# Kernel optimization log

Measured on AMD Instinct MI355X. Metric: run time of the kernel, lower is better.

Reference implementation:

```python
import jax, jax.numpy as jnp
import numpy as np

B, S = 32, 128          # batch, seq_len
C, K = 256, 128         # num_concept, dim_k (== dim_e == dim_correct)
DC = 128                # dim_correct
NQ, NIT, NUT = 10000, 1024, 1024


def _xavier(k, shape):
    fan_out, fan_in = shape[0], shape[1]
    bound = float(np.sqrt(6.0 / (fan_in + fan_out)))
    return jax.random.uniform(k, shape, jnp.float32, -bound, bound)


def setup_inputs() -> dict:
    key = jax.random.key(0)
    ks = jax.random.split(key, 16)
    question_seq = jax.random.randint(ks[0], (B, S), 0, NQ + 1)
    interval_time_seq = jax.random.randint(ks[1], (B, S), 0, NIT + 1)
    use_time_seq = jax.random.randint(ks[2], (B, S), 0, NUT + 1)
    correct_seq = jnp.round(jax.random.uniform(ks[3], (B, S))).astype(jnp.float32)
    E_q = _xavier(ks[4], (NQ + 1, K))
    E_it = _xavier(ks[5], (NIT + 1, K))
    E_ut = _xavier(ks[6], (NUT + 1, K))
    q_matrix = (jax.random.uniform(ks[7], (NQ + 1, C)) < 0.03).astype(jnp.float32)
    h0 = _xavier(ks[8], (C, K))  # xavier init of the initial concept memory
    W1 = _xavier(ks[9], (K, K + K + DC)); b1 = jnp.zeros((K,), jnp.float32)
    W2 = _xavier(ks[10], (K, 4 * K));     b2 = jnp.zeros((K,), jnp.float32)
    W3 = _xavier(ks[11], (K, 4 * K));     b3 = jnp.zeros((K,), jnp.float32)
    W4 = _xavier(ks[12], (K, 3 * K));     b4 = jnp.zeros((K,), jnp.float32)
    W5 = _xavier(ks[13], (K, 2 * K));     b5 = jnp.zeros((K,), jnp.float32)
    return dict(question_seq=question_seq, interval_time_seq=interval_time_seq,
                use_time_seq=use_time_seq, correct_seq=correct_seq,
                E_q=E_q, E_it=E_it, E_ut=E_ut, q_matrix=q_matrix, h0=h0,
                W1=W1, b1=b1, W2=W2, b2=b2, W3=W3, b3=b3,
                W4=W4, b4=b4, W5=W5, b5=b5)


def _forward(question_seq, interval_time_seq, use_time_seq, correct_seq,
             E_q, E_it, E_ut, q_matrix, h0,
             W1, b1, W2, b2, W3, b3, W4, b4, W5, b5):
    bsz, slen = question_seq.shape
    dim_k = h0.shape[1]
    dim_c = W1.shape[1] - 2 * dim_k

    q_emb = E_q[question_seq]            # [B,S,K]
    it_emb = E_it[interval_time_seq]     # [B,S,K]
    ut_emb = E_ut[use_time_seq]          # [B,S,K]
    c_emb = jnp.broadcast_to(correct_seq[..., None], (bsz, slen, dim_c))
    all_learning = jnp.concatenate([q_emb, ut_emb, c_emb], -1) @ W1.T + b1  # [B,S,K]
    qe = q_matrix[question_seq]          # [B,S,C]

    h_pre0 = jnp.tile(h0[None], (bsz, 1, 1))                     # [B,C,K]
    h_tilde0 = jnp.einsum('bc,bck->bk', qe[:, 0], h_pre0)        # q_e @ h at t=0
    learning0 = jnp.zeros((bsz, dim_k), all_learning.dtype)

    # split linear_4 weight over its (h_pre, LG, it) concat blocks
    W4h, W4l, W4i = W4[:, :dim_k], W4[:, dim_k:2 * dim_k], W4[:, 2 * dim_k:]

    # time-major per-step inputs for t = 0 .. S-2
    xs = (jnp.swapaxes(it_emb[:, :-1], 0, 1),
          jnp.swapaxes(all_learning[:, :-1], 0, 1),
          jnp.swapaxes(qe[:, :-1], 0, 1),
          jnp.swapaxes(qe[:, 1:], 0, 1),
          jnp.swapaxes(q_emb[:, 1:], 0, 1))

    def step(carry, x):
        h_pre, h_tilde_pre, learning_pre = carry
        it, learning, qe_t, qe_n, qemb_n = x
        cat = jnp.concatenate([learning_pre, it, learning, h_tilde_pre], -1)  # [B,4K]
        learning_gain = jnp.tanh(cat @ W2.T + b2)
        gamma_l = jax.nn.sigmoid(cat @ W3.T + b3)
        LG = gamma_l * (learning_gain + 1.0) * 0.5                 # [B,K]
        LG_tilde = qe_t[:, :, None] * LG[:, None, :]               # [B,C,K] outer write
        gamma_f = jax.nn.sigmoid(jnp.einsum('bck,jk->bcj', h_pre, W4h)
                                 + (LG @ W4l.T + it @ W4i.T + b4)[:, None, :])
        h = LG_tilde + gamma_f * h_pre                             # [B,C,K]
        h_tilde = jnp.einsum('bc,bck->bk', qe_n, h)                # read for t+1
        y = jax.nn.sigmoid(jnp.concatenate([qemb_n, h_tilde], -1) @ W5.T + b5).sum(-1) / dim_k
        return (h, h_tilde, learning), y

    _, ys = jax.lax.scan(step, (h_pre0, h_tilde0, learning0), xs)  # ys: [S-1,B]
    pred = jnp.concatenate([jnp.zeros((bsz, 1), ys.dtype), ys.T], axis=1)
    return pred


def reference(question_seq, interval_time_seq, use_time_seq, correct_seq,
              E_q, E_it, E_ut, q_matrix, h0,
              W1, b1, W2, b2, W3, b3, W4, b4, W5, b5):
    return _forward(question_seq, interval_time_seq, use_time_seq, correct_seq,
                    E_q, E_it, E_ut, q_matrix, h0,
                    W1, b1, W2, b2, W3, b3, W4, b4, W5, b5)
```

## Files before the change

kernel.cpp:

```cpp
#include <hip/hip_runtime.h>
#include <hip/hip_bf16.h>


typedef __bf16 bf16x8 __attribute__((ext_vector_type(8)));
typedef __bf16 bf16x4 __attribute__((ext_vector_type(4)));
typedef float f32x4 __attribute__((ext_vector_type(4)));

#define HBIDX(c,k) ((((c)<<7)) + ((k) ^ (((c)&15)<<3)))

__device__ __forceinline__ float sigmf(float x){
  return __builtin_amdgcn_rcpf(1.0f + __expf(-x));
}

__device__ __forceinline__ bf16x8 cvt8(float4 a, float4 b){
  bf16x8 r;
  r[0]=(__bf16)a.x; r[1]=(__bf16)a.y; r[2]=(__bf16)a.z; r[3]=(__bf16)a.w;
  r[4]=(__bf16)b.x; r[5]=(__bf16)b.y; r[6]=(__bf16)b.z; r[7]=(__bf16)b.w;
  return r;
}

__device__ __forceinline__ void mk_hilo(float4 a, float4 b, bf16x8& hi, bf16x8& lo){
  float v[8] = {a.x,a.y,a.z,a.w,b.x,b.y,b.z,b.w};
  #pragma unroll
  for (int i = 0; i < 8; i++){
    __bf16 h = (__bf16)v[i];
    hi[i] = h;
    lo[i] = (__bf16)(v[i] - (float)h);
  }
}

__device__ __forceinline__ f32x4 mfma16(bf16x8 a, bf16x8 b, f32x4 c){
  return __builtin_amdgcn_mfma_f32_16x16x32_bf16(a, b, c, 0, 0, 0);
}

__global__ __launch_bounds__(256) void k1_al(
    const int* __restrict__ qseq, const int* __restrict__ utseq,
    const float* __restrict__ corr,
    const float* __restrict__ Eq, const float* __restrict__ Eut,
    const float* __restrict__ W1, const float* __restrict__ b1,
    const float* __restrict__ W5, const float* __restrict__ b5,
    float* __restrict__ AL, float* __restrict__ pre5)
{
  __shared__ __bf16 inA[64*256];
  __shared__ float corrs[64];
  __shared__ float b1s[128], b5s[128], rsp[256];
  const int tid = threadIdx.x, blk = blockIdx.x;
  if (tid < 128){ b1s[tid]=b1[tid]; b5s[tid]=b5[tid]; }
  {
    int j = tid & 127, hf = tid >> 7;
    const float* p = W1 + j*384 + 256 + hf*64;
    float s = 0.f;
    for (int i = 0; i < 64; i++) s += p[i];
    rsp[tid] = s;
  }
  {
    int r = tid >> 2, seg = tid & 3;
    int R = blk*64 + r;
    int qi = qseq[R], ui = utseq[R];
    if (seg == 0) corrs[r] = corr[R];
    for (int i = 0; i < 64; i++){
      int col = seg*64 + i;
      float v = (col < 128) ? Eq[qi*128 + col] : Eut[ui*128 + (col-128)];
      inA[((r*256 + col) ^ ((r&7)<<3))] = (__bf16)v;
    }
  }
  __syncthreads();
  const int w = tid >> 6, lane = tid & 63;
  const int la = lane & 15, g = lane >> 4;
  const int rbase = w*16;
  bf16x8 af[8];
  #pragma unroll
  for (int kt = 0; kt < 8; kt++){
    int idx = ((rbase+la)*256 + kt*32 + g*8) ^ ((la&7)<<3);
    af[kt] = *(const bf16x8*)&inA[idx];
  }
  for (int jt = 0; jt < 8; jt++){
    f32x4 acc = {0.f,0.f,0.f,0.f};
    const float* Wb = W1 + (jt*16+la)*384;
    #pragma unroll
    for (int kt = 0; kt < 8; kt++){
      const float* p = Wb + kt*32 + g*8;
      acc = mfma16(af[kt], cvt8(*(const float4*)p, *(const float4*)(p+4)), acc);
    }
    int j = jt*16 + la;
    float rsj = rsp[j] + rsp[j+128];
    #pragma unroll
    for (int rr = 0; rr < 4; rr++){
      int row = rbase + g*4 + rr;
      int R = blk*64 + row;
      AL[R*128 + j] = acc[rr] + b1s[j] + corrs[row]*rsj;
    }
  }
  for (int jt = 0; jt < 8; jt++){
    f32x4 acc = {0.f,0.f,0.f,0.f};
    const float* Wb = W5 + (jt*16+la)*256;
    #pragma unroll
    for (int kt = 0; kt < 4; kt++){
      const float* p = Wb + kt*32 + g*8;
      acc = mfma16(af[kt], cvt8(*(const float4*)p, *(const float4*)(p+4)), acc);
    }
    int j = jt*16 + la;
    #pragma unroll
    for (int rr = 0; rr < 4; rr++){
      int row = rbase + g*4 + rr;
      int R = blk*64 + row;
      pre5[R*128 + j] = acc[rr] + b5s[j];
    }
  }
}

__global__ __launch_bounds__(256) void k2_pre(
    const int* __restrict__ itseq, const float* __restrict__ Eit,
    const float* __restrict__ AL,
    const float* __restrict__ W2, const float* __restrict__ W3,
    const float* __restrict__ W4,
    const float* __restrict__ b2, const float* __restrict__ b3,
    const float* __restrict__ b4,
    float* __restrict__ pre23, float* __restrict__ pre4)
{
  __shared__ __bf16 inA[64*384];
  __shared__ int obase[64];
  __shared__ float b2s[128], b3s[128], b4s[128];
  const int tid = threadIdx.x, blk = blockIdx.x;
  if (tid < 128){ b2s[tid]=b2[tid]; b3s[tid]=b3[tid]; b4s[tid]=b4[tid]; }
  {
    int r = tid >> 2, seg = tid & 3;
    int R = blk*64 + r;
    bool valid = (R < 4064);
    int b_ = R / 127, tau = R % 127;
    if (seg == 0) obase[r] = valid ? (b_*127 + tau) : -1;
    int itv = valid ? itseq[b_*128 + tau] : 0;
    for (int i = 0; i < 96; i++){
      int col = seg*96 + i;
      float v = 0.f;
      if (valid){
        if (col < 128)      v = (tau > 0) ? AL[(b_*128 + tau-1)*128 + col] : 0.f;
        else if (col < 256) v = Eit[itv*128 + (col-128)];
        else                v = AL[(b_*128 + tau)*128 + (col-256)];
      }
      inA[((r*384 + col) ^ ((r&7)<<3))] = (__bf16)v;
    }
  }
  __syncthreads();
  const int w = tid >> 6, lane = tid & 63;
  const int la = lane & 15, g = lane >> 4;
  const int rbase = w*16;
  bf16x8 af[12];
  #pragma unroll
  for (int kt = 0; kt < 12; kt++){
    int idx = ((rbase+la)*384 + kt*32 + g*8) ^ ((la&7)<<3);
    af[kt] = *(const bf16x8*)&inA[idx];
  }
  for (int jt = 0; jt < 16; jt++){
    f32x4 acc = {0.f,0.f,0.f,0.f};
    int j = jt*16 + la;
    const float* Wb = (j < 128) ? (W2 + j*512) : (W3 + (j-128)*512);
    #pragma unroll
    for (int kt = 0; kt < 12; kt++){
      const float* p = Wb + kt*32 + g*8;
      acc = mfma16(af[kt], cvt8(*(const float4*)p, *(const float4*)(p+4)), acc);
    }
    float bias = (j < 128) ? b2s[j] : b3s[j-128];
    #pragma unroll
    for (int rr = 0; rr < 4; rr++){
      int row = rbase + g*4 + rr;
      int ob = obase[row];
      if (ob >= 0) pre23[ob*256 + j] = acc[rr] + bias;
    }
  }
  for (int jt = 0; jt < 8; jt++){
    f32x4 acc = {0.f,0.f,0.f,0.f};
    int j = jt*16 + la;
    const float* Wb = W4 + j*384 + 256;
    #pragma unroll
    for (int kk = 0; kk < 4; kk++){
      const float* p = Wb + kk*32 + g*8;
      acc = mfma16(af[4+kk], cvt8(*(const float4*)p, *(const float4*)(p+4)), acc);
    }
    #pragma unroll
    for (int rr = 0; rr < 4; rr++){
      int row = rbase + g*4 + rr;
      int ob = obase[row];
      if (ob >= 0) pre4[ob*128 + j] = acc[rr] + b4s[j];
    }
  }
}

#define SCAN_LDS_BYTES (34944*4)

__global__ __launch_bounds__(512, 2) void lpkt_scan(
    const float* __restrict__ qmat, const int* __restrict__ qseq,
    const float* __restrict__ h0,
    const float* __restrict__ W2, const float* __restrict__ W3,
    const float* __restrict__ W4,
    const float* __restrict__ pre23, const float* __restrict__ pre4,
    float* __restrict__ hist)
{
  extern __shared__ float lds[];
  __bf16* hB  = (__bf16*)lds;
  float* htb0 = lds + 32768;
  float* htb1 = lds + 32896;
  float* LGb  = lds + 33024;
  float* zb   = lds + 33152;
  float* qeb  = lds + 33280;
  float* p23L = lds + 34048;
  float* p4L  = lds + 34560;
  int*   qsl  = (int*)(lds + 34816);

  const int tid  = threadIdx.x;
  const int b    = blockIdx.x;
  const int lane = tid & 63;
  const int w    = tid >> 6;
  const int la   = lane & 15, g = lane >> 4;
  const int jq   = w & 3;
  const int ch   = w >> 2;

  bf16x8 af[2][4];
  #pragma unroll
  for (int jj = 0; jj < 2; jj++){
    #pragma unroll
    for (int kt = 0; kt < 4; kt++){
      const float* p = W4 + ((jq*2+jj)*16+la)*384 + kt*32 + g*8;
      af[jj][kt] = cvt8(*(const float4*)p, *(const float4*)(p+4));
    }
  }
  bf16x8 af23[2][4];
  bf16x8 af4l[4];
  #pragma unroll
  for (int kt = 0; kt < 4; kt++){
    const float* p2 = W2 + (w*16+la)*512 + 384 + kt*32 + g*8;
    const float* p3 = W3 + (w*16+la)*512 + 384 + kt*32 + g*8;
    const float* p4 = W4 + (w*16+la)*384 + 128 + kt*32 + g*8;
    af23[0][kt] = cvt8(*(const float4*)p2, *(const float4*)(p2+4));
    af23[1][kt] = cvt8(*(const float4*)p3, *(const float4*)(p3+4));
    af4l[kt]    = cvt8(*(const float4*)p4, *(const float4*)(p4+4));
  }

  if (tid < 128) qsl[tid] = qseq[b*128 + tid];
  __syncthreads();
  const float* pre23b = pre23 + b*127*256;
  const float* pre4b  = pre4  + b*127*128;
  if (tid < 64)       *(float4*)&qeb[tid*4] = *(const float4*)(qmat + (size_t)qsl[0]*256 + tid*4);
  else if (tid < 128) *(float4*)&qeb[256 + (tid-64)*4] = *(const float4*)(qmat + (size_t)qsl[1]*256 + (tid-64)*4);
  else if (tid < 192) *(float4*)&p23L[(tid-128)*4] = *(const float4*)(pre23b + (tid-128)*4);
  else if (tid < 224) *(float4*)&p4L[(tid-192)*4]  = *(const float4*)(pre4b  + (tid-192)*4);
  else if (tid < 256){ float4 z4i = {0.f,0.f,0.f,0.f}; *(float4*)&htb0[(tid-224)*4] = z4i; }

  float4 hreg[8][2];
  #pragma unroll
  for (int cg = 0; cg < 8; cg++){
    const int c_ = ch*128 + cg*16 + la;
    #pragma unroll
    for (int jj = 0; jj < 2; jj++){
      const int k0 = (jq*2+jj)*16 + g*4;
      float4 v = *(const float4*)(h0 + c_*128 + k0);
      hreg[cg][jj] = v;
      bf16x4 hb; hb[0]=(__bf16)v.x; hb[1]=(__bf16)v.y; hb[2]=(__bf16)v.z; hb[3]=(__bf16)v.w;
      *(bf16x4*)&hB[HBIDX(c_, k0)] = hb;
    }
  }
  __syncthreads();
  #pragma unroll
  for (int cg = 0; cg < 8; cg++){
    const int c_ = ch*128 + cg*16 + la;
    float q = qeb[c_];
    if (q != 0.f){
      #pragma unroll
      for (int jj = 0; jj < 2; jj++){
        const int k0 = (jq*2+jj)*16 + g*4;
        float4 hv = hreg[cg][jj];
        atomicAdd(&htb0[k0+0], q*hv.x);
        atomicAdd(&htb0[k0+1], q*hv.y);
        atomicAdd(&htb0[k0+2], q*hv.z);
        atomicAdd(&htb0[k0+3], q*hv.w);
      }
    }
  }
  __syncthreads();

  int i0 = 0, i1 = 1, i2 = 2;

  for (int tau = 0; tau < 127; tau++){
    float* htc = (tau & 1) ? htb1 : htb0;
    float* htn = (tau & 1) ? htb0 : htb1;
    float* qec = qeb + i0*256;
    float* qen = qeb + i1*256;
    float* qep = qeb + i2*256;
    const float* p23c = p23L + (tau & 1)*256;
    const float* p4c  = p4L  + (tau & 1)*128;
    const __bf16* hBr = hB + (tau & 1)*32768;
    __bf16*       hBw = hB + ((tau+1) & 1)*32768;

    if (tid < 128) htn[tid] = 0.f;
    {
      bf16x8 xh[4], xl[4];
      #pragma unroll
      for (int kt = 0; kt < 4; kt++){
        int k0 = kt*32 + g*8;
        mk_hilo(*(const float4*)&htc[k0], *(const float4*)&htc[k0+4], xh[kt], xl[kt]);
      }
      f32x4 aLh = {0.f,0.f,0.f,0.f}, aLl = {0.f,0.f,0.f,0.f};
      f32x4 aGh = {0.f,0.f,0.f,0.f}, aGl = {0.f,0.f,0.f,0.f};
      #pragma unroll
      for (int kt = 0; kt < 4; kt++){
        aLh = mfma16(af23[0][kt], xh[kt], aLh);
        aLl = mfma16(af23[0][kt], xl[kt], aLl);
        aGh = mfma16(af23[1][kt], xh[kt], aGh);
        aGl = mfma16(af23[1][kt], xl[kt], aGl);
      }
      if (la == 0){
        float4 lp4 = *(const float4*)&p23c[w*16 + g*4];
        float4 gp4 = *(const float4*)&p23c[128 + w*16 + g*4];
        float4 LG4;
        LG4.x = sigmf(aGh[0]+aGl[0]+gp4.x) * sigmf(2.f*(aLh[0]+aLl[0]+lp4.x));
        LG4.y = sigmf(aGh[1]+aGl[1]+gp4.y) * sigmf(2.f*(aLh[1]+aLl[1]+lp4.y));
        LG4.z = sigmf(aGh[2]+aGl[2]+gp4.z) * sigmf(2.f*(aLh[2]+aLl[2]+lp4.z));
        LG4.w = sigmf(aGh[3]+aGl[3]+gp4.w) * sigmf(2.f*(aLh[3]+aLl[3]+lp4.w));
        *(float4*)&LGb[w*16 + g*4] = LG4;
      }
    }
    __syncthreads();

    {
      bf16x8 lh[4];
      #pragma unroll
      for (int kt = 0; kt < 4; kt++){
        int k0 = kt*32 + g*8;
        lh[kt] = cvt8(*(const float4*)&LGb[k0], *(const float4*)&LGb[k0+4]);
      }
      f32x4 az0 = {0.f,0.f,0.f,0.f}, az1 = {0.f,0.f,0.f,0.f};
      az0 = mfma16(af4l[0], lh[0], az0);
      az1 = mfma16(af4l[1], lh[1], az1);
      az0 = mfma16(af4l[2], lh[2], az0);
      az1 = mfma16(af4l[3], lh[3], az1);
      if (la == 0){
        float4 zp = *(const float4*)&p4c[w*16 + g*4];
        float4 zv = {az0[0]+az1[0]+zp.x, az0[1]+az1[1]+zp.y,
                     az0[2]+az1[2]+zp.z, az0[3]+az1[3]+zp.w};
        *(float4*)&zb[w*16 + g*4] = zv;
      }
    }
    __syncthreads();

    float4 pf23, pf4, pfqe;
    const bool dopf = (tau < 126);
    const bool do23 = dopf && (tid < 64);
    const bool do4  = dopf && (tid >= 64) && (tid < 96);
    const bool doqe = dopf && (tid >= 448);
    if (do23) pf23 = *(const float4*)(pre23b + (tau+1)*256 + tid*4);
    if (do4)  pf4  = *(const float4*)(pre4b  + (tau+1)*128 + (tid-64)*4);
    if (doqe) pfqe = *(const float4*)(qmat + (size_t)qsl[tau+2]*256 + (tid-448)*4);

    float4 z4[2], lg4[2];
    #pragma unroll
    for (int jj = 0; jj < 2; jj++){
      const int k0 = (jq*2+jj)*16 + g*4;
      z4[jj]  = *(const float4*)&zb[k0];
      lg4[jj] = *(const float4*)&LGb[k0];
    }

    #pragma unroll
    for (int cg = 0; cg < 8; cg++){
      const int c_ = ch*128 + cg*16 + la;
      bf16x8 bfv[4];
      #pragma unroll
      for (int kt = 0; kt < 4; kt++)
        bfv[kt] = *(const bf16x8*)&hBr[HBIDX(c_, kt*32 + g*8)];
      const float qe_t = qec[c_], qe_n = qen[c_];
      const bool nz = (qe_n != 0.f);
      #pragma unroll
      for (int jj = 0; jj < 2; jj++){
        f32x4 acc = {0.f,0.f,0.f,0.f};
        #pragma unroll
        for (int kt = 0; kt < 4; kt++)
          acc = mfma16(af[jj][kt], bfv[kt], acc);
        const int k0 = (jq*2+jj)*16 + g*4;
        float4 hp = hreg[cg][jj];
        float4 hn;
        hn.x = qe_t*lg4[jj].x + sigmf(acc[0] + z4[jj].x)*hp.x;
        hn.y = qe_t*lg4[jj].y + sigmf(acc[1] + z4[jj].y)*hp.y;
        hn.z = qe_t*lg4[jj].z + sigmf(acc[2] + z4[jj].z)*hp.z;
        hn.w = qe_t*lg4[jj].w + sigmf(acc[3] + z4[jj].w)*hp.w;
        hreg[cg][jj] = hn;
        bf16x4 hb; hb[0]=(__bf16)hn.x; hb[1]=(__bf16)hn.y; hb[2]=(__bf16)hn.z; hb[3]=(__bf16)hn.w;
        *(bf16x4*)&hBw[HBIDX(c_, k0)] = hb;
        if (nz){
          atomicAdd(&htn[k0+0], qe_n*hn.x);
          atomicAdd(&htn[k0+1], qe_n*hn.y);
          atomicAdd(&htn[k0+2], qe_n*hn.z);
          atomicAdd(&htn[k0+3], qe_n*hn.w);
        }
      }
    }
    if (do23) *(float4*)&p23L[((tau+1)&1)*256 + tid*4] = pf23;
    if (do4)  *(float4*)&p4L[((tau+1)&1)*128 + (tid-64)*4] = pf4;
    if (doqe) *(float4*)&qep[(tid-448)*4] = pfqe;
    __syncthreads();

    if (tid < 32){
      float4 v = *(const float4*)&htn[tid*4];
      *(float4*)(hist + ((size_t)b*127 + tau)*128 + tid*4) = v;
    }
    int t_ = i0; i0 = i1; i1 = i2; i2 = t_;
  }
}

__global__ __launch_bounds__(128) void k4_y(
    const float* __restrict__ hist, const float* __restrict__ pre5,
    const float* __restrict__ W5, float* __restrict__ out)
{
  const int R = blockIdx.x;
  const int s = R & 127, b = R >> 7;
  const int j = threadIdx.x;
  __shared__ float xs[128];
  __shared__ float partial[2];
  if (s == 0){ if (j == 0) out[R] = 0.f; return; }
  xs[j] = hist[((size_t)b*127 + (s-1))*128 + j];
  __syncthreads();
  const float* wr = W5 + j*256 + 128;
  float acc = pre5[(size_t)R*128 + j];
  #pragma unroll
  for (int k = 0; k < 128; k += 4){
    float4 wv = *(const float4*)&wr[k];
    float4 xv = *(const float4*)&xs[k];
    acc += wv.x*xv.x + wv.y*xv.y + wv.z*xv.z + wv.w*xv.w;
  }
  float v = sigmf(acc);
  #pragma unroll
  for (int m = 1; m < 64; m <<= 1) v += __shfl_xor(v, m);
  if ((j & 63) == 0) partial[j >> 6] = v;
  __syncthreads();
  if (j == 0) out[R] = (partial[0] + partial[1]) * (1.f/128.f);
}

extern "C" void kernel_launch(void* const* d_in, const int* in_sizes, int n_in,
                              void* d_out, int out_size, void* d_ws, size_t ws_size,
                              hipStream_t stream) {
  const int*   qseq  = (const int*)  d_in[0];
  const int*   itseq = (const int*)  d_in[1];
  const int*   utseq = (const int*)  d_in[2];
  const float* corr  = (const float*)d_in[3];
  const float* Eq    = (const float*)d_in[4];
  const float* Eit   = (const float*)d_in[5];
  const float* Eut   = (const float*)d_in[6];
  const float* qmat  = (const float*)d_in[7];
  const float* h0    = (const float*)d_in[8];
  const float* W1    = (const float*)d_in[9];
  const float* b1    = (const float*)d_in[10];
  const float* W2    = (const float*)d_in[11];
  const float* b2    = (const float*)d_in[12];
  const float* W3    = (const float*)d_in[13];
  const float* b3    = (const float*)d_in[14];
  const float* W4    = (const float*)d_in[15];
  const float* b4    = (const float*)d_in[16];
  const float* W5    = (const float*)d_in[17];
  const float* b5    = (const float*)d_in[18];
  float* out = (float*)d_out;

  float* ws    = (float*)d_ws;
  float* AL    = ws;
  float* hist  = ws;
  float* pre5  = ws + 524288;
  float* pre23 = ws + 1048576;
  float* pre4  = ws + 2088960;

  (void)hipFuncSetAttribute(reinterpret_cast<const void*>(&lpkt_scan),
                            hipFuncAttributeMaxDynamicSharedMemorySize,
                            SCAN_LDS_BYTES);

  hipLaunchKernelGGL(k1_al, dim3(64), dim3(256), 0, stream,
                     qseq, utseq, corr, Eq, Eut, W1, b1, W5, b5, AL, pre5);
  hipLaunchKernelGGL(k2_pre, dim3(64), dim3(256), 0, stream,
                     itseq, Eit, AL, W2, W3, W4, b2, b3, b4, pre23, pre4);
  hipLaunchKernelGGL(lpkt_scan, dim3(32), dim3(512), SCAN_LDS_BYTES, stream,
                     qmat, qseq, h0, W2, W3, W4, pre23, pre4, hist);
  hipLaunchKernelGGL(k4_y, dim3(4096), dim3(128), 0, stream,
                     hist, pre5, W5, out);
}
```

Before: 903.7 us.

## Remove a barrier per scan step and reduce h_tilde via shuffles

The z = W4l·LG matvec no longer runs as its own phase behind a barrier. Each wave now computes its own slice of z redundantly from a bf16 copy of LG, which drops one __syncthreads per timestep. The per-element atomicAdds into h_tilde, previously made only for nonzero q entries, are replaced by register accumulation, a 16-lane xor-shuffle reduction and a few atomics per wave. This costs extra MFMA work, extra weight registers and shuffles every step in exchange for fewer barriers and less LDS atomic contention.

Result: no change. 904.1 us (+0.0%).

```diff
diff --git a/kernel.cpp b/kernel.cpp
--- a/kernel.cpp
+++ b/kernel.cpp
@@ -31,6 +31,16 @@
 
 __device__ __forceinline__ f32x4 mfma16(bf16x8 a, bf16x8 b, f32x4 c){
   return __builtin_amdgcn_mfma_f32_16x16x32_bf16(a, b, c, 0, 0, 0);
+}
+
+__device__ __forceinline__ void red16(f32x4& r){
+  #pragma unroll
+  for (int m = 1; m < 16; m <<= 1){
+    r[0] += __shfl_xor(r[0], m);
+    r[1] += __shfl_xor(r[1], m);
+    r[2] += __shfl_xor(r[2], m);
+    r[3] += __shfl_xor(r[3], m);
+  }
 }
 
 __global__ __launch_bounds__(256) void k1_al(
@@ -186,7 +196,7 @@
   }
 }
 
-#define SCAN_LDS_BYTES (34944*4)
+#define SCAN_LDS_BYTES (34880*4)
 
 __global__ __launch_bounds__(512, 2) void lpkt_scan(
     const float* __restrict__ qmat, const int* __restrict__ qseq,
@@ -198,14 +208,14 @@
 {
   extern __shared__ float lds[];
   __bf16* hB  = (__bf16*)lds;
-  float* htb0 = lds + 32768;
-  float* htb1 = lds + 32896;
-  float* LGb  = lds + 33024;
-  float* zb   = lds + 33152;
-  float* qeb  = lds + 33280;
-  float* p23L = lds + 34048;
-  float* p4L  = lds + 34560;
-  int*   qsl  = (int*)(lds + 34816);
+  float*  htb0 = lds + 32768;
+  float*  htb1 = lds + 32896;
+  float*  LGb  = lds + 33024;
+  __bf16* LGh  = (__bf16*)(lds + 33152);
+  float*  qeb  = lds + 33216;
+  float*  p23L = lds + 33984;
+  float*  p4L  = lds + 34496;
+  int*    qsl  = (int*)(lds + 34752);
 
   const int tid  = threadIdx.x;
   const int b    = blockIdx.x;
@@ -216,24 +226,24 @@
   const int ch   = w >> 2;
 
   bf16x8 af[2][4];
+  bf16x8 af4l[2][4];
   #pragma unroll
   for (int jj = 0; jj < 2; jj++){
     #pragma unroll
     for (int kt = 0; kt < 4; kt++){
-      const float* p = W4 + ((jq*2+jj)*16+la)*384 + kt*32 + g*8;
-      af[jj][kt] = cvt8(*(const float4*)p, *(const float4*)(p+4));
+      const float* ph = W4 + ((jq*2+jj)*16+la)*384 + kt*32 + g*8;
+      const float* pl = W4 + ((jq*2+jj)*16+la)*384 + 128 + kt*32 + g*8;
+      af[jj][kt]   = cvt8(*(const float4*)ph, *(const float4*)(ph+4));
+      af4l[jj][kt] = cvt8(*(const float4*)pl, *(const float4*)(pl+4));
     }
   }
   bf16x8 af23[2][4];
-  bf16x8 af4l[4];
   #pragma unroll
   for (int kt = 0; kt < 4; kt++){
     const float* p2 = W2 + (w*16+la)*512 + 384 + kt*32 + g*8;
     const float* p3 = W3 + (w*16+la)*512 + 384 + kt*32 + g*8;
-    const float* p4 = W4 + (w*16+la)*384 + 128 + kt*32 + g*8;
     af23[0][kt] = cvt8(*(const float4*)p2, *(const float4*)(p2+4));
     af23[1][kt] = cvt8(*(const float4*)p3, *(const float4*)(p3+4));
-    af4l[kt]    = cvt8(*(const float4*)p4, *(const float4*)(p4+4));
   }
 
   if (tid < 128) qsl[tid] = qseq[b*128 + tid];
@@ -260,20 +270,23 @@
     }
   }
   __syncthreads();
-  #pragma unroll
-  for (int cg = 0; cg < 8; cg++){
-    const int c_ = ch*128 + cg*16 + la;
-    float q = qeb[c_];
-    if (q != 0.f){
-      #pragma unroll
-      for (int jj = 0; jj < 2; jj++){
-        const int k0 = (jq*2+jj)*16 + g*4;
-        float4 hv = hreg[cg][jj];
-        atomicAdd(&htb0[k0+0], q*hv.x);
-        atomicAdd(&htb0[k0+1], q*hv.y);
-        atomicAdd(&htb0[k0+2], q*hv.z);
-        atomicAdd(&htb0[k0+3], q*hv.w);
-      }
+  {
+    f32x4 r0 = {0.f,0.f,0.f,0.f}, r1 = {0.f,0.f,0.f,0.f};
+    #pragma unroll
+    for (int cg = 0; cg < 8; cg++){
+      const int c_ = ch*128 + cg*16 + la;
+      float q = qeb[c_];
+      float4 h0v = hreg[cg][0], h1v = hreg[cg][1];
+      r0[0] += q*h0v.x; r0[1] += q*h0v.y; r0[2] += q*h0v.z; r0[3] += q*h0v.w;
+      r1[0] += q*h1v.x; r1[1] += q*h1v.y; r1[2] += q*h1v.z; r1[3] += q*h1v.w;
+    }
+    red16(r0); red16(r1);
+    if (la == 0){
+      const int k0 = (jq*2)*16 + g*4, k1 = (jq*2+1)*16 + g*4;
+      atomicAdd(&htb0[k0+0], r0[0]); atomicAdd(&htb0[k0+1], r0[1]);
+      atomicAdd(&htb0[k0+2], r0[2]); atomicAdd(&htb0[k0+3], r0[3]);
+      atomicAdd(&htb0[k1+0], r1[0]); atomicAdd(&htb0[k1+1], r1[1]);
+      atomicAdd(&htb0[k1+2], r1[2]); atomicAdd(&htb0[k1+3], r1[3]);
     }
   }
   __syncthreads();
@@ -308,36 +321,19 @@
         aGh = mfma16(af23[1][kt], xh[kt], aGh);
         aGl = mfma16(af23[1][kt], xl[kt], aGl);
       }
+      float4 lp4 = *(const float4*)&p23c[w*16 + g*4];
+      float4 gp4 = *(const float4*)&p23c[128 + w*16 + g*4];
+      float4 LG4;
+      LG4.x = sigmf(aGh[0]+aGl[0]+gp4.x) * sigmf(2.f*(aLh[0]+aLl[0]+lp4.x));
+      LG4.y = sigmf(aGh[1]+aGl[1]+gp4.y) * sigmf(2.f*(aLh[1]+aLl[1]+lp4.y));
+      LG4.z = sigmf(aGh[2]+aGl[2]+gp4.z) * sigmf(2.f*(aLh[2]+aLl[2]+lp4.z));
+      LG4.w = sigmf(aGh[3]+aGl[3]+gp4.w) * sigmf(2.f*(aLh[3]+aLl[3]+lp4.w));
       if (la == 0){
-        float4 lp4 = *(const float4*)&p23c[w*16 + g*4];
-        float4 gp4 = *(const float4*)&p23c[128 + w*16 + g*4];
-        float4 LG4;
-        LG4.x = sigmf(aGh[0]+aGl[0]+gp4.x) * sigmf(2.f*(aLh[0]+aLl[0]+lp4.x));
-        LG4.y = sigmf(aGh[1]+aGl[1]+gp4.y) * sigmf(2.f*(aLh[1]+aLl[1]+lp4.y));
-        LG4.z = sigmf(aGh[2]+aGl[2]+gp4.z) * sigmf(2.f*(aLh[2]+aLl[2]+lp4.z));
-        LG4.w = sigmf(aGh[3]+aGl[3]+gp4.w) * sigmf(2.f*(aLh[3]+aLl[3]+lp4.w));
         *(float4*)&LGb[w*16 + g*4] = LG4;
-      }
-    }
-    __syncthreads();
-
-    {
-      bf16x8 lh[4];
-      #pragma unroll
-      for (int kt = 0; kt < 4; kt++){
-        int k0 = kt*32 + g*8;
-        lh[kt] = cvt8(*(const float4*)&LGb[k0], *(const float4*)&LGb[k0+4]);
-      }
-      f32x4 az0 = {0.f,0.f,0.f,0.f}, az1 = {0.f,0.f,0.f,0.f};
-      az0 = mfma16(af4l[0], lh[0], az0);
-      az1 = mfma16(af4l[1], lh[1], az1);
-      az0 = mfma16(af4l[2], lh[2], az0);
-      az1 = mfma16(af4l[3], lh[3], az1);
-      if (la == 0){
-        float4 zp = *(const float4*)&p4c[w*16 + g*4];
-        float4 zv = {az0[0]+az1[0]+zp.x, az0[1]+az1[1]+zp.y,
-                     az0[2]+az1[2]+zp.z, az0[3]+az1[3]+zp.w};
-        *(float4*)&zb[w*16 + g*4] = zv;
+        bf16x4 lgp;
+        lgp[0]=(__bf16)LG4.x; lgp[1]=(__bf16)LG4.y;
+        lgp[2]=(__bf16)LG4.z; lgp[3]=(__bf16)LG4.w;
+        *(bf16x4*)&LGh[w*16 + g*4] = lgp;
       }
     }
     __syncthreads();
@@ -351,14 +347,29 @@
     if (do4)  pf4  = *(const float4*)(pre4b  + (tau+1)*128 + (tid-64)*4);
     if (doqe) pfqe = *(const float4*)(qmat + (size_t)qsl[tau+2]*256 + (tid-448)*4);
 
-    float4 z4[2], lg4[2];
-    #pragma unroll
-    for (int jj = 0; jj < 2; jj++){
-      const int k0 = (jq*2+jj)*16 + g*4;
-      z4[jj]  = *(const float4*)&zb[k0];
-      lg4[jj] = *(const float4*)&LGb[k0];
-    }
-
+    float4 z4[2];
+    {
+      bf16x8 lh[4];
+      #pragma unroll
+      for (int kt = 0; kt < 4; kt++)
+        lh[kt] = *(const bf16x8*)&LGh[kt*32 + g*8];
+      #pragma unroll
+      for (int jj = 0; jj < 2; jj++){
+        f32x4 az = {0.f,0.f,0.f,0.f};
+        #pragma unroll
+        for (int kt = 0; kt < 4; kt++)
+          az = mfma16(af4l[jj][kt], lh[kt], az);
+        float4 zp = *(const float4*)&p4c[(jq*2+jj)*16 + g*4];
+        z4[jj].x = az[0]+zp.x; z4[jj].y = az[1]+zp.y;
+        z4[jj].z = az[2]+zp.z; z4[jj].w = az[3]+zp.w;
+      }
+    }
+    float4 lg4[2];
+    #pragma unroll
+    for (int jj = 0; jj < 2; jj++)
+      lg4[jj] = *(const float4*)&LGb[(jq*2+jj)*16 + g*4];
+
+    f32x4 r0 = {0.f,0.f,0.f,0.f}, r1 = {0.f,0.f,0.f,0.f};
     #pragma unroll
     for (int cg = 0; cg < 8; cg++){
       const int c_ = ch*128 + cg*16 + la;
@@ -367,7 +378,6 @@
       for (int kt = 0; kt < 4; kt++)
         bfv[kt] = *(const bf16x8*)&hBr[HBIDX(c_, kt*32 + g*8)];
       const float qe_t = qec[c_], qe_n = qen[c_];
-      const bool nz = (qe_n != 0.f);
       #pragma unroll
       for (int jj = 0; jj < 2; jj++){
         f32x4 acc = {0.f,0.f,0.f,0.f};
@@ -384,13 +394,18 @@
         hreg[cg][jj] = hn;
         bf16x4 hb; hb[0]=(__bf16)hn.x; hb[1]=(__bf16)hn.y; hb[2]=(__bf16)hn.z; hb[3]=(__bf16)hn.w;
         *(bf16x4*)&hBw[HBIDX(c_, k0)] = hb;
-        if (nz){
-          atomicAdd(&htn[k0+0], qe_n*hn.x);
-          atomicAdd(&htn[k0+1], qe_n*hn.y);
-          atomicAdd(&htn[k0+2], qe_n*hn.z);
-          atomicAdd(&htn[k0+3], qe_n*hn.w);
-        }
-      }
+        f32x4& r = (jj == 0) ? r0 : r1;
+        r[0] += qe_n*hn.x; r[1] += qe_n*hn.y;
+        r[2] += qe_n*hn.z; r[3] += qe_n*hn.w;
+      }
+    }
+    red16(r0); red16(r1);
+    if (la == 0){
+      const int k0 = (jq*2)*16 + g*4, k1 = (jq*2+1)*16 + g*4;
+      atomicAdd(&htn[k0+0], r0[0]); atomicAdd(&htn[k0+1], r0[1]);
+      atomicAdd(&htn[k0+2], r0[2]); atomicAdd(&htn[k0+3], r0[3]);
+      atomicAdd(&htn[k1+0], r1[0]); atomicAdd(&htn[k1+1], r1[1]);
+      atomicAdd(&htn[k1+2], r1[2]); atomicAdd(&htn[k1+3], r1[3]);
     }
     if (do23) *(float4*)&p23L[((tau+1)&1)*256 + tid*4] = pf23;
     if (do4)  *(float4*)&p4L[((tau+1)&1)*128 + (tid-64)*4] = pf4;
```
